# Optimization experiments

Hardware: AMD Instinct MI355X
Metric: run time of the kernel (lower is better)

The kernel has to match this reference:

```python
import jax, jax.numpy as jnp
import numpy as np

D_MODEL = 1024
NUM_HEADS = 16
HEAD_DIM = D_MODEL // NUM_HEADS


def setup_inputs() -> dict:
    key = jax.random.key(0)
    ks = jax.random.split(key, 10)
    B, SQ, SKV = 2, 2048, 2048
    s = 1.0 / np.sqrt(D_MODEL)
    inp = {
        "query": jax.random.normal(ks[0], (B, SQ, D_MODEL), jnp.float32),
        "key_value": jax.random.normal(ks[1], (B, SKV, D_MODEL), jnp.float32),
        "Wq": jax.random.normal(ks[2], (D_MODEL, D_MODEL), jnp.float32) * s,
        "bq": jnp.zeros((D_MODEL,), jnp.float32),
        "Wk": jax.random.normal(ks[3], (D_MODEL, D_MODEL), jnp.float32) * s,
        "bk": jnp.zeros((D_MODEL,), jnp.float32),
        "Wv": jax.random.normal(ks[4], (D_MODEL, D_MODEL), jnp.float32) * s,
        "bv": jnp.zeros((D_MODEL,), jnp.float32),
        "Wo": jax.random.normal(ks[5], (D_MODEL, D_MODEL), jnp.float32) * s,
        "bo": jnp.zeros((D_MODEL,), jnp.float32),
    }
    return inp


def reference(query, key_value, Wq, bq, Wk, bk, Wv, bv, Wo, bo):
    B, SQ, _ = query.shape
    SKV = key_value.shape[1]
    # projections (torch Linear: x @ W^T + b)
    Q = query @ Wq.T + bq
    K = key_value @ Wk.T + bk
    V = key_value @ Wv.T + bv
    # [B, H, S, Dh]
    Q = Q.reshape(B, SQ, NUM_HEADS, HEAD_DIM).transpose(0, 2, 1, 3)
    K = K.reshape(B, SKV, NUM_HEADS, HEAD_DIM).transpose(0, 2, 1, 3)
    V = V.reshape(B, SKV, NUM_HEADS, HEAD_DIM).transpose(0, 2, 1, 3)
    scores = jnp.einsum("bhqd,bhkd->bhqk", Q, K) / np.sqrt(HEAD_DIM)
    # causal mask: position q may attend to kv positions <= q
    causal = jnp.tril(jnp.ones((SQ, SKV), bool))  # True = keep
    scores = jnp.where(causal[None, None], scores, -jnp.inf)
    attn = jax.nn.softmax(scores, axis=-1)
    # dropout is identity in eval mode
    out = jnp.einsum("bhqk,bhkd->bhqd", attn, V)
    out = out.transpose(0, 2, 1, 3).reshape(B, SQ, D_MODEL)
    return out @ Wo.T + bo
```

## Files before the change

kernel.cpp:

```cpp
#include <hip/hip_runtime.h>
#include <hip/hip_bf16.h>
#include <cstdint>
#include <type_traits>

#define DM 1024
#define HEADS 16
#define DH 64
#define SEQ 2048
#define BATCH 2

typedef __attribute__((ext_vector_type(8))) short bf16x8;
typedef __attribute__((ext_vector_type(4))) float f32x4;
typedef __attribute__((ext_vector_type(16))) float f32x16;
typedef __attribute__((ext_vector_type(2))) unsigned int u32x2;
typedef __attribute__((ext_vector_type(4))) unsigned int u32x4;

#define SCALE2 0.18033688011112042f

static __device__ __forceinline__ unsigned short f2bf(float f) {
    unsigned u = __builtin_bit_cast(unsigned, f);
    u = u + 0x7fffu + ((u >> 16) & 1u);
    return (unsigned short)(u >> 16);
}

__global__ __launch_bounds__(256) void cast_all_k(
    const float* __restrict__ q, const float* __restrict__ kv,
    const float* __restrict__ wq, const float* __restrict__ wk,
    const float* __restrict__ wv, const float* __restrict__ wo,
    unsigned short* __restrict__ qb, unsigned short* __restrict__ kvb,
    unsigned short* __restrict__ wqb, unsigned short* __restrict__ wkb,
    unsigned short* __restrict__ wvb, unsigned short* __restrict__ wob)
{
    int blk = blockIdx.x;
    const float* s; unsigned short* d; int base;
    if (blk < 2048)      { s = q;  d = qb;  base = 0; }
    else if (blk < 4096) { s = kv; d = kvb; base = 2048; }
    else if (blk < 4608) { s = wq; d = wqb; base = 4096; }
    else if (blk < 5120) { s = wk; d = wkb; base = 4608; }
    else if (blk < 5632) { s = wv; d = wvb; base = 5120; }
    else                 { s = wo; d = wob; base = 5632; }
    int i = ((blk - base) * 256 + threadIdx.x) * 8;
    float4 a = *(const float4*)(s + i);
    float4 b2 = *(const float4*)(s + i + 4);
    ushort4 o0, o1;
    o0.x = f2bf(a.x);  o0.y = f2bf(a.y);  o0.z = f2bf(a.z);  o0.w = f2bf(a.w);
    o1.x = f2bf(b2.x); o1.y = f2bf(b2.y); o1.z = f2bf(b2.z); o1.w = f2bf(b2.w);
    *(ushort4*)(d + i) = o0;
    *(ushort4*)(d + i + 4) = o1;
}

template<int EPI>
__global__ __launch_bounds__(256) void gemm_nt(
    const unsigned short* __restrict__ A,
    const unsigned short* __restrict__ Bw,
    const float* __restrict__ biasA,
    const float* __restrict__ biasB,
    void* __restrict__ out0,
    void* __restrict__ out1,
    int M, int N, int K)
{
    constexpr int BK = 64;
    __shared__ alignas(16) unsigned short As[64 * BK];
    __shared__ alignas(16) unsigned short Bs[128 * BK];

    const int t = threadIdx.x;
    const int lane = t & 63;
    const int w = t >> 6;
    const int wn = w * 32;
    const int lr = lane & 15, lg = lane >> 4;
    const int m0 = blockIdx.x * 64, n0 = blockIdx.y * 128;

    f32x4 acc[4][2] = {};

    const int srow = t >> 3;
    const int schunk = t & 7;

    for (int kt = 0; kt < K; kt += BK) {
#pragma unroll
        for (int c = 0; c < 2; c++) {
            int row = srow + c * 32;
            int gc = schunk ^ (row & 7);
            __builtin_amdgcn_global_load_lds(
                (const __attribute__((address_space(1))) unsigned int*)(A + (size_t)(m0 + row) * K + kt + gc * 8),
                (__attribute__((address_space(3))) unsigned int*)(&As[row * BK + schunk * 8]), 16, 0, 0);
        }
#pragma unroll
        for (int c = 0; c < 4; c++) {
            int row = srow + c * 32;
            int gc = schunk ^ (row & 7);
            __builtin_amdgcn_global_load_lds(
                (const __attribute__((address_space(1))) unsigned int*)(Bw + (size_t)(n0 + row) * K + kt + gc * 8),
                (__attribute__((address_space(3))) unsigned int*)(&Bs[row * BK + schunk * 8]), 16, 0, 0);
        }
        __syncthreads();
#pragma unroll
        for (int kk = 0; kk < 2; kk++) {
            bf16x8 af[4], bfr[2];
#pragma unroll
            for (int i = 0; i < 4; i++)
                af[i] = *(const bf16x8*)(&As[(i * 16 + lr) * BK + (((kk * 4 + lg) ^ (lr & 7))) * 8]);
#pragma unroll
            for (int jj = 0; jj < 2; jj++)
                bfr[jj] = *(const bf16x8*)(&Bs[(wn + jj * 16 + lr) * BK + (((kk * 4 + lg) ^ (lr & 7))) * 8]);
#pragma unroll
            for (int i = 0; i < 4; i++)
#pragma unroll
                for (int jj = 0; jj < 2; jj++)
                    acc[i][jj] = __builtin_amdgcn_mfma_f32_16x16x32_bf16(af[i], bfr[jj], acc[i][jj], 0, 0, 0);
        }
        __syncthreads();
    }

    if constexpr (EPI == 0) {
        unsigned short* C = (unsigned short*)out0;
#pragma unroll
        for (int i = 0; i < 4; i++) {
            int rbase = m0 + i * 16 + lg * 4;
#pragma unroll
            for (int jj = 0; jj < 2; jj++) {
                int col = n0 + wn + jj * 16 + lr;
                float bv = biasA[col];
#pragma unroll
                for (int r = 0; r < 4; r++)
                    C[(size_t)(rbase + r) * 1024 + col] = f2bf((acc[i][jj][r] + bv) * SCALE2);
            }
        }
    } else if constexpr (EPI == 1) {
        if (n0 < 1024) {
            unsigned short* C = (unsigned short*)out0;
#pragma unroll
            for (int i = 0; i < 4; i++) {
                int rbase = m0 + i * 16 + lg * 4;
#pragma unroll
                for (int jj = 0; jj < 2; jj++) {
                    int col = n0 + wn + jj * 16 + lr;
                    float bv = biasA[col];
#pragma unroll
                    for (int r = 0; r < 4; r++)
                        C[(size_t)(rbase + r) * 1024 + col] = f2bf(acc[i][jj][r] + bv);
                }
            }
        } else {
            unsigned short* C = (unsigned short*)out1;
            int bidx = m0 >> 11;
#pragma unroll
            for (int i = 0; i < 4; i++) {
                int s0 = (m0 & 2047) + i * 16 + lg * 4;
#pragma unroll
                for (int jj = 0; jj < 2; jj++) {
                    int nv = n0 - 1024 + wn + jj * 16 + lr;
                    float bv = biasB[nv];
                    int hh = nv >> 6, dd = nv & 63;
                    ushort4 st;
                    st.x = f2bf(acc[i][jj][0] + bv);
                    st.y = f2bf(acc[i][jj][1] + bv);
                    st.z = f2bf(acc[i][jj][2] + bv);
                    st.w = f2bf(acc[i][jj][3] + bv);
                    *(ushort4*)(C + ((size_t)((bidx * HEADS + hh) * DH + dd)) * SEQ + s0) = st;
                }
            }
        }
    } else {
        float* C = (float*)out0;
#pragma unroll
        for (int i = 0; i < 4; i++) {
            int rbase = m0 + i * 16 + lg * 4;
#pragma unroll
            for (int jj = 0; jj < 2; jj++) {
                int col = n0 + wn + jj * 16 + lr;
                float bv = biasA[col];
#pragma unroll
                for (int r = 0; r < 4; r++)
                    C[(size_t)(rbase + r) * 1024 + col] = acc[i][jj][r] + bv;
            }
        }
    }
}

__global__ __launch_bounds__(512, 2) void attn_k(
    const unsigned short* __restrict__ Qp,
    const unsigned short* __restrict__ Kp,
    const unsigned short* __restrict__ Vt,
    unsigned short* __restrict__ Ctx)
{
    const int lane = threadIdx.x & 63;
    const int w = threadIdx.x >> 6;
    const int x = blockIdx.x;
    const int j = x >> 5;
    const int bh = x & 31;
    const int b = bh >> 4, h = bh & 15;
    const int qt = (w < 4) ? (j * 4 + w) : (63 - j * 4 - (w & 3));
    const int q0 = qt * 32;
    const int lq = lane & 31;
    const int hi = lane >> 5;
    const int qq = q0 + lq;
    const int nb = (qt >> 1) + 1;
    constexpr float THR = 11.5f;

    bf16x8 Qf[4];
    {
        const unsigned short* qb = Qp + (size_t)(b * SEQ + qq) * DM + h * DH + hi * 8;
#pragma unroll
        for (int d = 0; d < 4; d++) Qf[d] = *(const bf16x8*)(qb + d * 16);
    }

    const unsigned short* kbase = Kp + ((size_t)(b * SEQ + lq)) * DM + h * DH + hi * 8;
    const unsigned short* vbase = Vt + ((size_t)((b * HEADS + h) * DH) + lq) * SEQ + hi * 8;

    f32x16 o0 = {}, o1 = {};
    float m_run = -1e30f, l_run = 0.f;
    bf16x8 KA[4], KB[4];

    {
#pragma unroll
        for (int d = 0; d < 4; d++) {
            KA[d] = *(const bf16x8*)(kbase + d * 16);
            KB[d] = *(const bf16x8*)(kbase + (size_t)32 * DM + d * 16);
        }
    }

    const int qmh0 = qq - 4 * hi;

    auto body = [&](int ib, auto PF) {
        constexpr bool pf = PF.value;
        const int kb = ib * 64;

        bf16x8 Vc[4][2];
        {
            const unsigned short* vp = vbase + kb;
#pragma unroll
            for (int s = 0; s < 4; s++)
#pragma unroll
                for (int dt = 0; dt < 2; dt++)
                    Vc[s][dt] = *(const bf16x8*)(vp + (size_t)dt * 32 * SEQ + s * 16);
        }
        bf16x8 KnA[4], KnB[4];
        if constexpr (pf) {
            const unsigned short* kp = kbase + (size_t)(kb + 64) * DM;
#pragma unroll
            for (int d = 0; d < 4; d++) {
                KnA[d] = *(const bf16x8*)(kp + d * 16);
                KnB[d] = *(const bf16x8*)(kp + (size_t)32 * DM + d * 16);
            }
        }

        f32x16 sa0 = {}, sa1 = {};
#pragma unroll
        for (int d = 0; d < 4; d++) {
            sa0 = __builtin_amdgcn_mfma_f32_32x32x16_bf16(KA[d], Qf[d], sa0, 0, 0, 0);
            sa1 = __builtin_amdgcn_mfma_f32_32x32x16_bf16(KB[d], Qf[d], sa1, 0, 0, 0);
        }

        const int qmh = qmh0 - kb;
#pragma unroll
        for (int r = 0; r < 16; r++) {
            int kvl = (r & 3) + 8 * (r >> 2);
            sa0[r] = (kvl <= qmh) ? sa0[r] : -1e30f;
            sa1[r] = (kvl + 32 <= qmh) ? sa1[r] : -1e30f;
        }
        float mx[16];
#pragma unroll
        for (int r = 0; r < 16; r++) mx[r] = fmaxf(sa0[r], sa1[r]);
#pragma unroll
        for (int r = 0; r < 8; r++) mx[r] = fmaxf(mx[r], mx[r + 8]);
#pragma unroll
        for (int r = 0; r < 4; r++) mx[r] = fmaxf(mx[r], mx[r + 4]);
        mx[0] = fmaxf(mx[0], mx[2]);
        mx[1] = fmaxf(mx[1], mx[3]);
        float mloc = fmaxf(mx[0], mx[1]);
        mloc = fmaxf(mloc, __shfl_xor(mloc, 32));

        if (!__all(mloc - m_run <= THR)) {
            float m_new = fmaxf(m_run, mloc);
            float sf = __builtin_amdgcn_exp2f(m_run - m_new);
            l_run *= sf;
#pragma unroll
            for (int r = 0; r < 16; r++) { o0[r] *= sf; o1[r] *= sf; }
            m_run = m_new;
        }

        float p0v[16], p1v[16];
#pragma unroll
        for (int r = 0; r < 16; r++) {
            p0v[r] = __builtin_amdgcn_exp2f(sa0[r] - m_run);
            p1v[r] = __builtin_amdgcn_exp2f(sa1[r] - m_run);
        }
        float s4[8];
#pragma unroll
        for (int r = 0; r < 8; r++) s4[r] = (p0v[r] + p0v[r + 8]) + (p1v[r] + p1v[r + 8]);
#pragma unroll
        for (int r = 0; r < 4; r++) s4[r] += s4[r + 4];
        float ps = (s4[0] + s4[1]) + (s4[2] + s4[3]);
        ps += __shfl_xor(ps, 32);
        l_run += ps;

        unsigned c0[8], c1[8];
#pragma unroll
        for (int i = 0; i < 8; i++) {
            unsigned pk;
            asm("v_cvt_pk_bf16_f32 %0, %1, %2" : "=v"(pk) : "v"(p0v[2 * i]), "v"(p0v[2 * i + 1]));
            c0[i] = pk;
            asm("v_cvt_pk_bf16_f32 %0, %1, %2" : "=v"(pk) : "v"(p1v[2 * i]), "v"(p1v[2 * i + 1]));
            c1[i] = pk;
        }
        bf16x8 Pb[4];
        {
            u32x2 r02 = __builtin_amdgcn_permlane32_swap(c0[0], c0[2], false, false);
            u32x2 r13 = __builtin_amdgcn_permlane32_swap(c0[1], c0[3], false, false);
            u32x2 r46 = __builtin_amdgcn_permlane32_swap(c0[4], c0[6], false, false);
            u32x2 r57 = __builtin_amdgcn_permlane32_swap(c0[5], c0[7], false, false);
            u32x4 w0 = {r02.x, r13.x, r02.y, r13.y};
            u32x4 w1 = {r46.x, r57.x, r46.y, r57.y};
            Pb[0] = __builtin_bit_cast(bf16x8, w0);
            Pb[1] = __builtin_bit_cast(bf16x8, w1);
        }
        {
            u32x2 r02 = __builtin_amdgcn_permlane32_swap(c1[0], c1[2], false, false);
            u32x2 r13 = __builtin_amdgcn_permlane32_swap(c1[1], c1[3], false, false);
            u32x2 r46 = __builtin_amdgcn_permlane32_swap(c1[4], c1[6], false, false);
            u32x2 r57 = __builtin_amdgcn_permlane32_swap(c1[5], c1[7], false, false);
            u32x4 w0 = {r02.x, r13.x, r02.y, r13.y};
            u32x4 w1 = {r46.x, r57.x, r46.y, r57.y};
            Pb[2] = __builtin_bit_cast(bf16x8, w0);
            Pb[3] = __builtin_bit_cast(bf16x8, w1);
        }

#pragma unroll
        for (int s = 0; s < 4; s++) {
            o0 = __builtin_amdgcn_mfma_f32_32x32x16_bf16(Vc[s][0], Pb[s], o0, 0, 0, 0);
            o1 = __builtin_amdgcn_mfma_f32_32x32x16_bf16(Vc[s][1], Pb[s], o1, 0, 0, 0);
        }

        if constexpr (pf) {
#pragma unroll
            for (int d = 0; d < 4; d++) { KA[d] = KnA[d]; KB[d] = KnB[d]; }
        }
    };

    for (int ib = 0; ib + 1 < nb; ib++)
        body(ib, std::true_type{});
    body(nb - 1, std::false_type{});

    float inv = 1.0f / l_run;
    unsigned short* cb = Ctx + (size_t)(b * SEQ + qq) * DM + h * DH + hi * 4;
#pragma unroll
    for (int g = 0; g < 4; g++) {
        ushort4 s0, s1;
        s0.x = f2bf(o0[4 * g + 0] * inv); s0.y = f2bf(o0[4 * g + 1] * inv);
        s0.z = f2bf(o0[4 * g + 2] * inv); s0.w = f2bf(o0[4 * g + 3] * inv);
        s1.x = f2bf(o1[4 * g + 0] * inv); s1.y = f2bf(o1[4 * g + 1] * inv);
        s1.z = f2bf(o1[4 * g + 2] * inv); s1.w = f2bf(o1[4 * g + 3] * inv);
        *(ushort4*)(cb + g * 8) = s0;
        *(ushort4*)(cb + 32 + g * 8) = s1;
    }
}

extern "C" void kernel_launch(void* const* d_in, const int* in_sizes, int n_in,
                              void* d_out, int out_size, void* d_ws, size_t ws_size,
                              hipStream_t stream)
{
    const float* query = (const float*)d_in[0];
    const float* keyv  = (const float*)d_in[1];
    const float* Wq = (const float*)d_in[2];
    const float* bq = (const float*)d_in[3];
    const float* Wk = (const float*)d_in[4];
    const float* bk = (const float*)d_in[5];
    const float* Wv = (const float*)d_in[6];
    const float* bv = (const float*)d_in[7];
    const float* Wo = (const float*)d_in[8];
    const float* bo = (const float*)d_in[9];
    float* out = (float*)d_out;

    const int M = BATCH * SEQ;
    char* ws = (char*)d_ws;
    size_t off = 0;
    auto alloc = [&](size_t elems) { unsigned short* p = (unsigned short*)(ws + off); off += elems * 2; return p; };
    unsigned short* qb  = alloc((size_t)M * DM);
    unsigned short* kvb = alloc((size_t)M * DM);
    unsigned short* wqb = alloc((size_t)DM * DM);
    unsigned short* wkb = alloc((size_t)DM * DM);
    unsigned short* wvb = alloc((size_t)DM * DM);
    unsigned short* wob = alloc((size_t)DM * DM);
    unsigned short* Qp  = alloc((size_t)M * DM);
    unsigned short* Kp  = alloc((size_t)M * DM);
    unsigned short* Vt  = alloc((size_t)M * DM);
    unsigned short* Ctx = alloc((size_t)M * DM);

    cast_all_k<<<6144, 256, 0, stream>>>(query, keyv, Wq, Wk, Wv, Wo,
                                         qb, kvb, wqb, wkb, wvb, wob);

    gemm_nt<0><<<dim3(M / 64, 8),  256, 0, stream>>>(qb,  wqb, bq, nullptr, Qp, nullptr, M, DM, DM);
    gemm_nt<1><<<dim3(M / 64, 16), 256, 0, stream>>>(kvb, wkb, bk, bv,      Kp, Vt,      M, 2 * DM, DM);

    attn_k<<<dim3(256), 512, 0, stream>>>(Qp, Kp, Vt, Ctx);

    gemm_nt<2><<<dim3(M / 64, 8),  256, 0, stream>>>(Ctx, wob, bo, nullptr, out, nullptr, M, DM, DM);
}
```

Measured before the change: 137.3 us.

## Share K/V tiles across waves via double-buffered LDS async loads in attention

The attention kernel changes from each wave streaming its own K/V tiles from global memory into registers to a block of four waves covering a 128-row query chunk and sharing XOR-swizzled K/V tiles staged in LDS with global_load_lds double buffering. The grid becomes 512 blocks of 256 threads, and chunks are paired in a balanced order to even out causal work. This reduces redundant global/L2 traffic for K and V and overlaps the next tile's load with compute. In exchange it adds a __syncthreads per tile, and waves whose causal range ends early sit idle while they wait at the barrier.

```diff
diff --git a/kernel.cpp b/kernel.cpp
--- a/kernel.cpp
+++ b/kernel.cpp
@@ -177,24 +177,27 @@
     }
 }
 
-__global__ __launch_bounds__(512, 2) void attn_k(
+__global__ __launch_bounds__(256, 2) void attn_k(
     const unsigned short* __restrict__ Qp,
     const unsigned short* __restrict__ Kp,
     const unsigned short* __restrict__ Vt,
     unsigned short* __restrict__ Ctx)
 {
+    __shared__ alignas(16) unsigned char ldsb[2 * 16384];
+
     const int lane = threadIdx.x & 63;
     const int w = threadIdx.x >> 6;
     const int x = blockIdx.x;
-    const int j = x >> 5;
     const int bh = x & 31;
+    const int i16 = x >> 5;
+    const int c = (i16 < 8) ? (2 * i16) : (31 - 2 * i16);
     const int b = bh >> 4, h = bh & 15;
-    const int qt = (w < 4) ? (j * 4 + w) : (63 - j * 4 - (w & 3));
-    const int q0 = qt * 32;
+    const int q0 = c * 128;
     const int lq = lane & 31;
     const int hi = lane >> 5;
-    const int qq = q0 + lq;
-    const int nb = (qt >> 1) + 1;
+    const int qq = q0 + w * 32 + lq;
+    const int nb = 2 * c + 2;
+    const int my_nb = (q0 + 32 * w + 95) >> 6;
     constexpr float THR = 11.5f;
 
     bf16x8 Qf[4];
@@ -204,142 +207,151 @@
         for (int d = 0; d < 4; d++) Qf[d] = *(const bf16x8*)(qb + d * 16);
     }
 
-    const unsigned short* kbase = Kp + ((size_t)(b * SEQ + lq)) * DM + h * DH + hi * 8;
-    const unsigned short* vbase = Vt + ((size_t)((b * HEADS + h) * DH) + lq) * SEQ + hi * 8;
+    const int colx = (((lane & 7) ^ (lane >> 3)) << 4);
+    const char* kg[2];
+    const char* vg[2];
+#pragma unroll
+    for (int u = 0; u < 2; u++) {
+        int s = 2 * w + u;
+        int row = 8 * s + (lane >> 3);
+        kg[u] = (const char*)Kp + (((size_t)(b * SEQ + row) * DM + h * DH) * 2) + colx;
+        vg[u] = (const char*)Vt + ((((size_t)(b * HEADS + h) * DH + row) * SEQ) * 2) + colx;
+    }
+    const int kxor = (lq & 7) << 4;
+
+    auto stage = [&](int buf, int t) {
+        int kboff_k = t * (64 * DM * 2);
+        int kboff_v = t * 128;
+#pragma unroll
+        for (int u = 0; u < 2; u++) {
+            int s = 2 * w + u;
+            __builtin_amdgcn_global_load_lds(
+                (const __attribute__((address_space(1))) unsigned int*)(kg[u] + kboff_k),
+                (__attribute__((address_space(3))) unsigned int*)(&ldsb[buf * 16384 + s * 1024 + lane * 16]), 16, 0, 0);
+            __builtin_amdgcn_global_load_lds(
+                (const __attribute__((address_space(1))) unsigned int*)(vg[u] + kboff_v),
+                (__attribute__((address_space(3))) unsigned int*)(&ldsb[buf * 16384 + 8192 + s * 1024 + lane * 16]), 16, 0, 0);
+        }
+    };
 
     f32x16 o0 = {}, o1 = {};
     float m_run = -1e30f, l_run = 0.f;
-    bf16x8 KA[4], KB[4];
-
-    {
-#pragma unroll
-        for (int d = 0; d < 4; d++) {
-            KA[d] = *(const bf16x8*)(kbase + d * 16);
-            KB[d] = *(const bf16x8*)(kbase + (size_t)32 * DM + d * 16);
-        }
-    }
-
     const int qmh0 = qq - 4 * hi;
 
-    auto body = [&](int ib, auto PF) {
-        constexpr bool pf = PF.value;
-        const int kb = ib * 64;
-
-        bf16x8 Vc[4][2];
-        {
-            const unsigned short* vp = vbase + kb;
+    stage(0, 0);
+    __syncthreads();
+
+    for (int t = 0; t < nb; t++) {
+        const int cur = t & 1;
+        if (t + 1 < nb) stage(cur ^ 1, t + 1);
+
+        if (t < my_nb) {
+            const unsigned char* Kb = &ldsb[cur * 16384];
+            const unsigned char* Vb = Kb + 8192;
+            const int kb = t * 64;
+
+            bf16x8 KA[4], KB[4], Vc[4][2];
+#pragma unroll
+            for (int d = 0; d < 4; d++) {
+                int col = (d * 32 + hi * 16) ^ kxor;
+                KA[d] = *(const bf16x8*)(Kb + lq * 128 + col);
+                KB[d] = *(const bf16x8*)(Kb + (lq + 32) * 128 + col);
+            }
 #pragma unroll
             for (int s = 0; s < 4; s++)
 #pragma unroll
                 for (int dt = 0; dt < 2; dt++)
-                    Vc[s][dt] = *(const bf16x8*)(vp + (size_t)dt * 32 * SEQ + s * 16);
-        }
-        bf16x8 KnA[4], KnB[4];
-        if constexpr (pf) {
-            const unsigned short* kp = kbase + (size_t)(kb + 64) * DM;
+                    Vc[s][dt] = *(const bf16x8*)(Vb + (dt * 32 + lq) * 128 + ((s * 32 + hi * 16) ^ kxor));
+
+            f32x16 sa0 = {}, sa1 = {};
 #pragma unroll
             for (int d = 0; d < 4; d++) {
-                KnA[d] = *(const bf16x8*)(kp + d * 16);
-                KnB[d] = *(const bf16x8*)(kp + (size_t)32 * DM + d * 16);
-            }
-        }
-
-        f32x16 sa0 = {}, sa1 = {};
-#pragma unroll
-        for (int d = 0; d < 4; d++) {
-            sa0 = __builtin_amdgcn_mfma_f32_32x32x16_bf16(KA[d], Qf[d], sa0, 0, 0, 0);
-            sa1 = __builtin_amdgcn_mfma_f32_32x32x16_bf16(KB[d], Qf[d], sa1, 0, 0, 0);
-        }
-
-        const int qmh = qmh0 - kb;
-#pragma unroll
-        for (int r = 0; r < 16; r++) {
-            int kvl = (r & 3) + 8 * (r >> 2);
-            sa0[r] = (kvl <= qmh) ? sa0[r] : -1e30f;
-            sa1[r] = (kvl + 32 <= qmh) ? sa1[r] : -1e30f;
-        }
-        float mx[16];
-#pragma unroll
-        for (int r = 0; r < 16; r++) mx[r] = fmaxf(sa0[r], sa1[r]);
-#pragma unroll
-        for (int r = 0; r < 8; r++) mx[r] = fmaxf(mx[r], mx[r + 8]);
-#pragma unroll
-        for (int r = 0; r < 4; r++) mx[r] = fmaxf(mx[r], mx[r + 4]);
-        mx[0] = fmaxf(mx[0], mx[2]);
-        mx[1] = fmaxf(mx[1], mx[3]);
-        float mloc = fmaxf(mx[0], mx[1]);
-        mloc = fmaxf(mloc, __shfl_xor(mloc, 32));
-
-        if (!__all(mloc - m_run <= THR)) {
-            float m_new = fmaxf(m_run, mloc);
-            float sf = __builtin_amdgcn_exp2f(m_run - m_new);
-            l_run *= sf;
-#pragma unroll
-            for (int r = 0; r < 16; r++) { o0[r] *= sf; o1[r] *= sf; }
-            m_run = m_new;
-        }
-
-        float p0v[16], p1v[16];
-#pragma unroll
-        for (int r = 0; r < 16; r++) {
-            p0v[r] = __builtin_amdgcn_exp2f(sa0[r] - m_run);
-            p1v[r] = __builtin_amdgcn_exp2f(sa1[r] - m_run);
-        }
-        float s4[8];
-#pragma unroll
-        for (int r = 0; r < 8; r++) s4[r] = (p0v[r] + p0v[r + 8]) + (p1v[r] + p1v[r + 8]);
-#pragma unroll
-        for (int r = 0; r < 4; r++) s4[r] += s4[r + 4];
-        float ps = (s4[0] + s4[1]) + (s4[2] + s4[3]);
-        ps += __shfl_xor(ps, 32);
-        l_run += ps;
-
-        unsigned c0[8], c1[8];
-#pragma unroll
-        for (int i = 0; i < 8; i++) {
-            unsigned pk;
-            asm("v_cvt_pk_bf16_f32 %0, %1, %2" : "=v"(pk) : "v"(p0v[2 * i]), "v"(p0v[2 * i + 1]));
-            c0[i] = pk;
-            asm("v_cvt_pk_bf16_f32 %0, %1, %2" : "=v"(pk) : "v"(p1v[2 * i]), "v"(p1v[2 * i + 1]));
-            c1[i] = pk;
-        }
-        bf16x8 Pb[4];
-        {
-            u32x2 r02 = __builtin_amdgcn_permlane32_swap(c0[0], c0[2], false, false);
-            u32x2 r13 = __builtin_amdgcn_permlane32_swap(c0[1], c0[3], false, false);
-            u32x2 r46 = __builtin_amdgcn_permlane32_swap(c0[4], c0[6], false, false);
-            u32x2 r57 = __builtin_amdgcn_permlane32_swap(c0[5], c0[7], false, false);
-            u32x4 w0 = {r02.x, r13.x, r02.y, r13.y};
-            u32x4 w1 = {r46.x, r57.x, r46.y, r57.y};
-            Pb[0] = __builtin_bit_cast(bf16x8, w0);
-            Pb[1] = __builtin_bit_cast(bf16x8, w1);
-        }
-        {
-            u32x2 r02 = __builtin_amdgcn_permlane32_swap(c1[0], c1[2], false, false);
-            u32x2 r13 = __builtin_amdgcn_permlane32_swap(c1[1], c1[3], false, false);
-            u32x2 r46 = __builtin_amdgcn_permlane32_swap(c1[4], c1[6], false, false);
-            u32x2 r57 = __builtin_amdgcn_permlane32_swap(c1[5], c1[7], false, false);
-            u32x4 w0 = {r02.x, r13.x, r02.y, r13.y};
-            u32x4 w1 = {r46.x, r57.x, r46.y, r57.y};
-            Pb[2] = __builtin_bit_cast(bf16x8, w0);
-            Pb[3] = __builtin_bit_cast(bf16x8, w1);
-        }
-
-#pragma unroll
-        for (int s = 0; s < 4; s++) {
-            o0 = __builtin_amdgcn_mfma_f32_32x32x16_bf16(Vc[s][0], Pb[s], o0, 0, 0, 0);
-            o1 = __builtin_amdgcn_mfma_f32_32x32x16_bf16(Vc[s][1], Pb[s], o1, 0, 0, 0);
-        }
-
-        if constexpr (pf) {
-#pragma unroll
-            for (int d = 0; d < 4; d++) { KA[d] = KnA[d]; KB[d] = KnB[d]; }
-        }
-    };
-
-    for (int ib = 0; ib + 1 < nb; ib++)
-        body(ib, std::true_type{});
-    body(nb - 1, std::false_type{});
+                sa0 = __builtin_amdgcn_mfma_f32_32x32x16_bf16(KA[d], Qf[d], sa0, 0, 0, 0);
+                sa1 = __builtin_amdgcn_mfma_f32_32x32x16_bf16(KB[d], Qf[d], sa1, 0, 0, 0);
+            }
+
+            const int qmh = qmh0 - kb;
+#pragma unroll
+            for (int r = 0; r < 16; r++) {
+                int kvl = (r & 3) + 8 * (r >> 2);
+                sa0[r] = (kvl <= qmh) ? sa0[r] : -1e30f;
+                sa1[r] = (kvl + 32 <= qmh) ? sa1[r] : -1e30f;
+            }
+            float mx[16];
+#pragma unroll
+            for (int r = 0; r < 16; r++) mx[r] = fmaxf(sa0[r], sa1[r]);
+#pragma unroll
+            for (int r = 0; r < 8; r++) mx[r] = fmaxf(mx[r], mx[r + 8]);
+#pragma unroll
+            for (int r = 0; r < 4; r++) mx[r] = fmaxf(mx[r], mx[r + 4]);
+            mx[0] = fmaxf(mx[0], mx[2]);
+            mx[1] = fmaxf(mx[1], mx[3]);
+            float mloc = fmaxf(mx[0], mx[1]);
+            mloc = fmaxf(mloc, __shfl_xor(mloc, 32));
+
+            if (!__all(mloc - m_run <= THR)) {
+                float m_new = fmaxf(m_run, mloc);
+                float sf = __builtin_amdgcn_exp2f(m_run - m_new);
+                l_run *= sf;
+#pragma unroll
+                for (int r = 0; r < 16; r++) { o0[r] *= sf; o1[r] *= sf; }
+                m_run = m_new;
+            }
+
+            float p0v[16], p1v[16];
+#pragma unroll
+            for (int r = 0; r < 16; r++) {
+                p0v[r] = __builtin_amdgcn_exp2f(sa0[r] - m_run);
+                p1v[r] = __builtin_amdgcn_exp2f(sa1[r] - m_run);
+            }
+            float s4[8];
+#pragma unroll
+            for (int r = 0; r < 8; r++) s4[r] = (p0v[r] + p0v[r + 8]) + (p1v[r] + p1v[r + 8]);
+#pragma unroll
+            for (int r = 0; r < 4; r++) s4[r] += s4[r + 4];
+            float ps = (s4[0] + s4[1]) + (s4[2] + s4[3]);
+            ps += __shfl_xor(ps, 32);
+            l_run += ps;
+
+            unsigned c0[8], c1[8];
+#pragma unroll
+            for (int ii = 0; ii < 8; ii++) {
+                unsigned pk;
+                asm("v_cvt_pk_bf16_f32 %0, %1, %2" : "=v"(pk) : "v"(p0v[2 * ii]), "v"(p0v[2 * ii + 1]));
+                c0[ii] = pk;
+                asm("v_cvt_pk_bf16_f32 %0, %1, %2" : "=v"(pk) : "v"(p1v[2 * ii]), "v"(p1v[2 * ii + 1]));
+                c1[ii] = pk;
+            }
+            bf16x8 Pb[4];
+            {
+                u32x2 r02 = __builtin_amdgcn_permlane32_swap(c0[0], c0[2], false, false);
+                u32x2 r13 = __builtin_amdgcn_permlane32_swap(c0[1], c0[3], false, false);
+                u32x2 r46 = __builtin_amdgcn_permlane32_swap(c0[4], c0[6], false, false);
+                u32x2 r57 = __builtin_amdgcn_permlane32_swap(c0[5], c0[7], false, false);
+                u32x4 w0 = {r02.x, r13.x, r02.y, r13.y};
+                u32x4 w1 = {r46.x, r57.x, r46.y, r57.y};
+                Pb[0] = __builtin_bit_cast(bf16x8, w0);
+                Pb[1] = __builtin_bit_cast(bf16x8, w1);
+            }
+            {
+                u32x2 r02 = __builtin_amdgcn_permlane32_swap(c1[0], c1[2], false, false);
+                u32x2 r13 = __builtin_amdgcn_permlane32_swap(c1[1], c1[3], false, false);
+                u32x2 r46 = __builtin_amdgcn_permlane32_swap(c1[4], c1[6], false, false);
+                u32x2 r57 = __builtin_amdgcn_permlane32_swap(c1[5], c1[7], false, false);
+                u32x4 w0 = {r02.x, r13.x, r02.y, r13.y};
+                u32x4 w1 = {r46.x, r57.x, r46.y, r57.y};
+                Pb[2] = __builtin_bit_cast(bf16x8, w0);
+                Pb[3] = __builtin_bit_cast(bf16x8, w1);
+            }
+
+#pragma unroll
+            for (int s = 0; s < 4; s++) {
+                o0 = __builtin_amdgcn_mfma_f32_32x32x16_bf16(Vc[s][0], Pb[s], o0, 0, 0, 0);
+                o1 = __builtin_amdgcn_mfma_f32_32x32x16_bf16(Vc[s][1], Pb[s], o1, 0, 0, 0);
+            }
+        }
+        __syncthreads();
+    }
 
     float inv = 1.0f / l_run;
     unsigned short* cb = Ctx + (size_t)(b * SEQ + qq) * DM + h * DH + hi * 4;
@@ -392,7 +404,7 @@
     gemm_nt<0><<<dim3(M / 64, 8),  256, 0, stream>>>(qb,  wqb, bq, nullptr, Qp, nullptr, M, DM, DM);
     gemm_nt<1><<<dim3(M / 64, 16), 256, 0, stream>>>(kvb, wkb, bk, bv,      Kp, Vt,      M, 2 * DM, DM);
 
-    attn_k<<<dim3(256), 512, 0, stream>>>(Qp, Kp, Vt, Ctx);
+    attn_k<<<dim3(512), 256, 0, stream>>>(Qp, Kp, Vt, Ctx);
 
     gemm_nt<2><<<dim3(M / 64, 8),  256, 0, stream>>>(Ctx, wob, bo, nullptr, out, nullptr, M, DM, DM);
 }
```

Result: faster. 121.1 us (-11.8%).
